# Optimization experiments

Hardware: AMD Instinct MI355X
Metric: run time of the kernel (lower is better)

## Reference

```python
import jax, jax.numpy as jnp
import numpy as np

N_TRAIN = 131072
M_TEST = 65536
T_SPAN = 100.0
D = 3  # Matern-5/2 state dim


def setup_inputs() -> dict:
    key = jax.random.key(0)
    k1, k2, k3, k4 = jax.random.split(key, 4)
    times = jnp.sort(jax.random.uniform(k1, (N_TRAIN,), jnp.float32) * T_SPAN)
    t_star = jnp.sort(jax.random.uniform(k2, (M_TEST,), jnp.float32) * T_SPAN)
    # positive site precisions, site naturals scaled so pseudo-targets are O(1)
    site_nat2 = jax.random.uniform(k3, (N_TRAIN,), jnp.float32) * 4.0 + 0.5
    site_nat1 = jax.random.normal(k4, (N_TRAIN,), jnp.float32) * site_nat2
    return dict(
        times=times,
        t_star=t_star,
        site_nat1=site_nat1,
        site_nat2=site_nat2,
        variance=jnp.float32(1.0),
        lengthscale=jnp.float32(0.5),
        mean_const=jnp.float32(0.1),
    )


def _matern52_sde(variance, lengthscale):
    lam = jnp.sqrt(5.0).astype(jnp.float32) / lengthscale
    F = jnp.array([[0.0, 1.0, 0.0],
                   [0.0, 0.0, 1.0],
                   [0.0, 0.0, 0.0]], jnp.float32)
    F = F.at[2, 0].set(-lam ** 3).at[2, 1].set(-3.0 * lam ** 2).at[2, 2].set(-3.0 * lam)
    kappa = lam ** 2 / 3.0
    P_inf = variance * jnp.array([[1.0, 0.0, 0.0],
                                  [0.0, 0.0, 0.0],
                                  [0.0, 0.0, 0.0]], jnp.float32)
    P_inf = P_inf.at[0, 2].set(-variance * kappa)
    P_inf = P_inf.at[2, 0].set(-variance * kappa)
    P_inf = P_inf.at[1, 1].set(variance * kappa)
    P_inf = P_inf.at[2, 2].set(variance * lam ** 4)
    H = jnp.array([[1.0, 0.0, 0.0]], jnp.float32)
    return F, H, P_inf, lam


def _discretise(F, P_inf, lam, dt):
    # (F + lam I) is nilpotent of index 3 -> exact expm
    I = jnp.eye(D, dtype=jnp.float32)
    Nm = F + lam * I
    Nm2 = Nm @ Nm
    dt_ = dt[:, None, None]
    A = jnp.exp(-lam * dt)[:, None, None] * (I + dt_ * Nm + 0.5 * dt_ ** 2 * Nm2)
    APA = jnp.einsum('tij,jk,tlk->til', A, P_inf, A)
    Q = P_inf - APA
    return A, Q


def _kalman_filter(H, P_inf, A_seq, Q_seq, residual, is_obs, R_full):
    h = H[0]  # [D]

    def step(carry, inp):
        m, P = carry
        A, Q, r, obs, R = inp
        m_pred = A @ m
        P_pred = A @ P @ A.T + Q
        S = h @ P_pred @ h + R
        K = obs * (P_pred @ h) / S  # masked gain: test points skip update
        v = r - m_pred @ h
        m_f = m_pred + K * v
        P_f = P_pred - jnp.outer(K, K) * S
        return (m_f, P_f), (m_pred, P_pred, m_f, P_f)

    init = (jnp.zeros(D, jnp.float32), P_inf)
    _, (m_pred, P_pred, m_filt, P_filt) = jax.lax.scan(
        step, init, (A_seq, Q_seq, residual, is_obs, R_full))
    return m_pred, P_pred, m_filt, P_filt


def _rts_smoother(m_pred, P_pred, m_filt, P_filt, A_seq):
    def back(carry, inp):
        m_s_next, P_s_next = carry
        m_f, P_f, A_n, m_p_n, P_p_n = inp
        G = jnp.linalg.solve(P_p_n, A_n @ P_f).T  # P_f A^T P_pred^{-1}
        m_s = m_f + G @ (m_s_next - m_p_n)
        P_s = P_f + G @ (P_s_next - P_p_n) @ G.T
        return (m_s, P_s), (m_s, P_s)

    init = (m_filt[-1], P_filt[-1])
    xs = (m_filt[:-1], P_filt[:-1], A_seq[1:], m_pred[1:], P_pred[1:])
    _, (m_s, P_s) = jax.lax.scan(back, init, xs, reverse=True)
    m_smooth = jnp.concatenate([m_s, m_filt[-1:]], axis=0)
    P_smooth = jnp.concatenate([P_s, P_filt[-1:]], axis=0)
    return m_smooth, P_smooth


def reference(times, t_star, site_nat1, site_nat2, variance, lengthscale, mean_const):
    F, H, P_inf, lam = _matern52_sde(variance, lengthscale)
    N = times.shape[0]
    M = t_star.shape[0]
    merged = jnp.concatenate([times, t_star])
    order = jnp.argsort(merged)  # jnp.argsort is stable
    merged_sorted = merged[order]
    is_obs = jnp.concatenate([jnp.ones(N, jnp.float32), jnp.zeros(M, jnp.float32)])[order]
    pseudo_targets = site_nat1 / site_nat2
    residual_full = jnp.concatenate([pseudo_targets - mean_const,
                                     jnp.zeros(M, jnp.float32)])[order]
    R_full = jnp.concatenate([jnp.reciprocal(site_nat2), jnp.ones(M, jnp.float32)])[order]
    dt_full = jnp.concatenate([jnp.zeros(1, jnp.float32), jnp.diff(merged_sorted)])
    A_seq, Q_seq = _discretise(F, P_inf, lam, dt_full)
    m_pred, P_pred, m_filt, P_filt = _kalman_filter(
        H, P_inf, A_seq, Q_seq, residual_full, is_obs, R_full)
    m_smooth, P_smooth = _rts_smoother(m_pred, P_pred, m_filt, P_filt, A_seq)
    inv_order = jnp.argsort(order)
    test_positions = inv_order[N:]
    m_test = m_smooth[test_positions]
    P_test = P_smooth[test_positions]
    means = m_test @ H[0] + mean_const  # H = [1,0,0]
    vars_ = jnp.einsum('i,tij,j->t', H[0], P_test, H[0])
    return means, jnp.maximum(vars_, 0.0)
```

## Files before the change

kernel.cpp:

```cpp
#include <hip/hip_runtime.h>
#include <math.h>

#define DEV __device__ __forceinline__

constexpr int N_TRAIN = 131072;
constexpr int M_TEST  = 65536;
constexpr int T_TOT   = N_TRAIN + M_TEST;
constexpr int CHUNK   = 4;
constexpr int NTH     = T_TOT / CHUNK;
constexpr int TPB     = 64;
constexpr int NBLK    = NTH / TPB;
constexpr int MIDT    = 256;
constexpr int FE_S    = 33;
constexpr int SE_S    = 19;

DEV int IDX4(int k) { return (k & (CHUNK - 1)) * NTH + (k >> 2); }

DEV void mm(const double* X, const double* Y, double* Z) {
#pragma unroll
  for (int i = 0; i < 3; ++i)
#pragma unroll
    for (int j = 0; j < 3; ++j)
      Z[i*3+j] = X[i*3]*Y[j] + X[i*3+1]*Y[3+j] + X[i*3+2]*Y[6+j];
}
DEV void mmnt(const double* X, const double* Y, double* Z) {
#pragma unroll
  for (int i = 0; i < 3; ++i)
#pragma unroll
    for (int j = 0; j < 3; ++j)
      Z[i*3+j] = X[i*3]*Y[j*3] + X[i*3+1]*Y[j*3+1] + X[i*3+2]*Y[j*3+2];
}
DEV void mtn(const double* X, const double* Y, double* Z) {
#pragma unroll
  for (int i = 0; i < 3; ++i)
#pragma unroll
    for (int j = 0; j < 3; ++j)
      Z[i*3+j] = X[i]*Y[j] + X[3+i]*Y[3+j] + X[6+i]*Y[6+j];
}
DEV void mv(const double* X, const double* v, double* w) {
#pragma unroll
  for (int i = 0; i < 3; ++i) w[i] = X[i*3]*v[0] + X[i*3+1]*v[1] + X[i*3+2]*v[2];
}
DEV void mtv(const double* X, const double* v, double* w) {
#pragma unroll
  for (int i = 0; i < 3; ++i) w[i] = X[i]*v[0] + X[3+i]*v[1] + X[6+i]*v[2];
}
DEV void inv3(const double* m, double* o) {
  double c00 = m[4]*m[8] - m[5]*m[7];
  double c10 = m[5]*m[6] - m[3]*m[8];
  double c20 = m[3]*m[7] - m[4]*m[6];
  double det = m[0]*c00 + m[1]*c10 + m[2]*c20;
  double id = 1.0 / det;
  o[0] = c00*id; o[1] = (m[2]*m[7]-m[1]*m[8])*id; o[2] = (m[1]*m[5]-m[2]*m[4])*id;
  o[3] = c10*id; o[4] = (m[0]*m[8]-m[2]*m[6])*id; o[5] = (m[2]*m[3]-m[0]*m[5])*id;
  o[6] = c20*id; o[7] = (m[1]*m[6]-m[0]*m[7])*id; o[8] = (m[0]*m[4]-m[1]*m[3])*id;
}
DEV void symm(double* P) {
  double a = 0.5*(P[1]+P[3]), b = 0.5*(P[2]+P[6]), c = 0.5*(P[5]+P[7]);
  P[1]=P[3]=a; P[2]=P[6]=b; P[5]=P[7]=c;
}

struct Model { double lam, v, kap, l4; };
DEV Model make_model(const float* varp, const float* ellp) {
  Model M; M.v = (double)varp[0];
  double ell = (double)ellp[0];
  M.lam = sqrt(5.0) / ell;
  M.kap = M.lam * M.lam / 3.0;
  double l2 = M.lam * M.lam;
  M.l4 = l2 * l2;
  return M;
}
DEV void pinf(const Model& M, double* P) {
  double vk = M.v * M.kap;
  P[0]=M.v; P[1]=0;  P[2]=-vk;
  P[3]=0;   P[4]=vk; P[5]=0;
  P[6]=-vk; P[7]=0;  P[8]=M.v*M.l4;
}
DEV void make_AQ(const Model& M, double dt, double* A, double* Q) {
  double lam = M.lam, l2 = lam*lam, l3 = l2*lam, l4 = M.l4;
  double e = (double)__expf((float)(-lam * dt));
  double h = 0.5 * dt * dt;
  A[0] = e*(1.0 + dt*lam + h*l2);
  A[1] = e*(dt + 2.0*h*lam);
  A[2] = e*h;
  A[3] = e*(-h*l3);
  A[4] = e*(1.0 + dt*lam - 2.0*h*l2);
  A[5] = e*(dt - h*lam);
  A[6] = e*(-dt*l3 + h*l4);
  A[7] = e*(-3.0*dt*l2 + 2.0*h*l3);
  A[8] = e*(1.0 - 2.0*dt*lam + h*l2);
  double vk = M.v * M.kap, vl4 = M.v * M.l4;
  double B[9];
#pragma unroll
  for (int i = 0; i < 3; ++i) {
    B[i*3+0] =  A[i*3+0]*M.v - A[i*3+2]*vk;
    B[i*3+1] =  A[i*3+1]*vk;
    B[i*3+2] = -A[i*3+0]*vk  + A[i*3+2]*vl4;
  }
  double Pi[9]; pinf(M, Pi);
#pragma unroll
  for (int i = 0; i < 3; ++i)
#pragma unroll
    for (int j = 0; j < 3; ++j)
      Q[i*3+j] = Pi[i*3+j] - (B[i*3]*A[j*3] + B[i*3+1]*A[j*3+1] + B[i*3+2]*A[j*3+2]);
}

struct FE { double A[9]; double b[3]; double C[9]; double h[3]; double J[9]; };

DEV FE fe_identity() {
  FE e;
#pragma unroll
  for (int i=0;i<9;++i){ e.A[i]=0.0; e.C[i]=0.0; e.J[i]=0.0; }
  e.A[0]=e.A[4]=e.A[8]=1.0;
  e.b[0]=e.b[1]=e.b[2]=0.0; e.h[0]=e.h[1]=e.h[2]=0.0;
  return e;
}
DEV void fe_store(const FE& e, double* g) {
#pragma unroll
  for (int i=0;i<9;++i) g[i]=e.A[i];
  g[9]=e.b[0]; g[10]=e.b[1]; g[11]=e.b[2];
#pragma unroll
  for (int i=0;i<9;++i) g[12+i]=e.C[i];
  g[21]=e.h[0]; g[22]=e.h[1]; g[23]=e.h[2];
#pragma unroll
  for (int i=0;i<9;++i) g[24+i]=e.J[i];
}
DEV FE fe_load(const double* g) {
  FE e;
#pragma unroll
  for (int i=0;i<9;++i) e.A[i]=g[i];
  e.b[0]=g[9]; e.b[1]=g[10]; e.b[2]=g[11];
#pragma unroll
  for (int i=0;i<9;++i) e.C[i]=g[12+i];
  e.h[0]=g[21]; e.h[1]=g[22]; e.h[2]=g[23];
#pragma unroll
  for (int i=0;i<9;++i) e.J[i]=g[24+i];
  return e;
}
DEV FE build_felem(const Model& M, double dt, float obsf, float rf, float Rf_, bool first) {
  FE E;
  double r = (double)rf, R = (double)Rf_;
  double g = (obsf > 0.5f) ? 1.0 : 0.0;
  if (first) {
#pragma unroll
    for (int i=0;i<9;++i){ E.A[i]=0.0; E.J[i]=0.0; }
    E.h[0]=E.h[1]=E.h[2]=0.0;
    double Pi[9]; pinf(M, Pi);
    double S = Pi[0] + R;
    double f = g / S;
    double K0=Pi[0]*f, K1=Pi[3]*f, K2=Pi[6]*f;
    E.b[0]=K0*r; E.b[1]=K1*r; E.b[2]=K2*r;
    E.C[0]=Pi[0]-S*K0*K0; E.C[1]=Pi[1]-S*K0*K1; E.C[2]=Pi[2]-S*K0*K2;
    E.C[3]=Pi[3]-S*K1*K0; E.C[4]=Pi[4]-S*K1*K1; E.C[5]=Pi[5]-S*K1*K2;
    E.C[6]=Pi[6]-S*K2*K0; E.C[7]=Pi[7]-S*K2*K1; E.C[8]=Pi[8]-S*K2*K2;
    return E;
  }
  double Am[9], Q[9]; make_AQ(M, dt, Am, Q);
  double S = Q[0] + R, iS = g / S;
  double K0=Q[0]*iS, K1=Q[3]*iS, K2=Q[6]*iS;
#pragma unroll
  for (int j = 0; j < 3; ++j) {
    E.A[j]   = Am[j]   - K0*Am[j];
    E.A[3+j] = Am[3+j] - K1*Am[j];
    E.A[6+j] = Am[6+j] - K2*Am[j];
    E.C[j]   = Q[j]    - K0*Q[j];
    E.C[3+j] = Q[3+j]  - K1*Q[j];
    E.C[6+j] = Q[6+j]  - K2*Q[j];
  }
  E.b[0]=K0*r; E.b[1]=K1*r; E.b[2]=K2*r;
  double riS = r*iS;
  E.h[0]=Am[0]*riS; E.h[1]=Am[1]*riS; E.h[2]=Am[2]*riS;
#pragma unroll
  for (int i = 0; i < 3; ++i)
#pragma unroll
    for (int j = 0; j < 3; ++j)
      E.J[i*3+j] = Am[i]*Am[j]*iS;
  return E;
}
DEV FE fcompose(const FE& x, const FE& y) {
  const double *A1=x.A,*b1=x.b,*C1=x.C,*h1=x.h,*J1=x.J;
  const double *A2=y.A,*b2=y.b,*C2=y.C,*h2=y.h,*J2=y.J;
  FE o;
  double Mx[9]; mm(C1,J2,Mx); Mx[0]+=1.0; Mx[4]+=1.0; Mx[8]+=1.0;
  double Mi[9]; inv3(Mx,Mi);
  double T1[9]; mm(A2,Mi,T1);
  mm(T1,A1,o.A);
  double u[3]; mv(C1,h2,u); u[0]+=b1[0]; u[1]+=b1[1]; u[2]+=b1[2];
  mv(T1,u,o.b); o.b[0]+=b2[0]; o.b[1]+=b2[1]; o.b[2]+=b2[2];
  double t2[9]; mm(T1,C1,t2);
  mmnt(t2,A2,o.C);
#pragma unroll
  for (int i=0;i<9;++i) o.C[i]+=C2[i];
  double tmp[9]; mm(Mi,A1,tmp);
  double w[3]; mv(J2,b1,w);
  w[0]=h2[0]-w[0]; w[1]=h2[1]-w[1]; w[2]=h2[2]-w[2];
  mtv(tmp,w,o.h); o.h[0]+=h1[0]; o.h[1]+=h1[1]; o.h[2]+=h1[2];
  double V[9]; mm(J2,A1,V);
  mtn(tmp,V,o.J);
#pragma unroll
  for (int i=0;i<9;++i) o.J[i]+=J1[i];
  symm(o.C); symm(o.J);
  return o;
}
DEV void fstep(const Model& M, double dt, float obsf, float rf, float Rf_,
               double* m, double* P) {
  double A[9], Q[9]; make_AQ(M, dt, A, Q);
  double mp[3]; mv(A, m, mp);
  double W[9]; mmnt(P, A, W);
  double Pp[9]; mm(A, W, Pp);
#pragma unroll
  for (int i=0;i<9;++i) Pp[i]+=Q[i];
  double S = Pp[0] + (double)Rf_;
  double f = (obsf > 0.5f) ? (1.0/S) : 0.0;
  double K0=Pp[0]*f, K1=Pp[3]*f, K2=Pp[6]*f;
  double v = (double)rf - mp[0];
  m[0]=mp[0]+K0*v; m[1]=mp[1]+K1*v; m[2]=mp[2]+K2*v;
  P[0]=Pp[0]-S*K0*K0; P[1]=Pp[1]-S*K0*K1; P[2]=Pp[2]-S*K0*K2;
  P[3]=Pp[3]-S*K1*K0; P[4]=Pp[4]-S*K1*K1; P[5]=Pp[5]-S*K1*K2;
  P[6]=Pp[6]-S*K2*K0; P[7]=Pp[7]-S*K2*K1; P[8]=Pp[8]-S*K2*K2;
  symm(P);
}

struct SE { double G[9]; double c[3]; double U[9]; };

DEV SE se_identity() {
  SE s;
#pragma unroll
  for (int i=0;i<9;++i){ s.G[i]=0.0; s.U[i]=0.0; }
  s.G[0]=s.G[4]=s.G[8]=1.0;
  s.c[0]=s.c[1]=s.c[2]=0.0;
  return s;
}
DEV void se_store(const SE& s, double* g) {
#pragma unroll
  for (int i=0;i<9;++i) g[i]=s.G[i];
  g[9]=s.c[0]; g[10]=s.c[1]; g[11]=s.c[2];
  g[12]=s.U[0]; g[13]=s.U[1]; g[14]=s.U[2]; g[15]=s.U[4]; g[16]=s.U[5]; g[17]=s.U[8];
}
DEV SE se_load(const double* g) {
  SE s;
#pragma unroll
  for (int i=0;i<9;++i) s.G[i]=g[i];
  s.c[0]=g[9]; s.c[1]=g[10]; s.c[2]=g[11];
  s.U[0]=g[12]; s.U[1]=g[13]; s.U[2]=g[14];
  s.U[3]=g[13]; s.U[4]=g[15]; s.U[5]=g[16];
  s.U[6]=g[14]; s.U[7]=g[16]; s.U[8]=g[17];
  return s;
}
DEV SE scompose(const SE& x, const SE& y) {
  SE o;
  mm(x.G, y.G, o.G);
  double t[3]; mv(x.G, y.c, t);
  o.c[0]=t[0]+x.c[0]; o.c[1]=t[1]+x.c[1]; o.c[2]=t[2]+x.c[2];
  double T[9]; mm(x.G, y.U, T);
  mmnt(T, x.G, o.U);
#pragma unroll
  for (int i=0;i<9;++i) o.U[i]+=x.U[i];
  symm(o.U);
  return o;
}
DEV void sapply(const SE& s, double* m, double* P) {
  double t[3]; mv(s.G, m, t);
  double T[9]; mm(s.G, P, T);
  double Pn[9]; mmnt(T, s.G, Pn);
  m[0]=t[0]+s.c[0]; m[1]=t[1]+s.c[1]; m[2]=t[2]+s.c[2];
#pragma unroll
  for (int i=0;i<9;++i) P[i]=Pn[i]+s.U[i];
  symm(P);
}
DEV SE build_selem(const Model& M, const float4* pk, const double* mf, const double* Pf,
                   int i, int t) {
  int ik  = i*NTH + t;
  int ik1 = (i < CHUNK-1) ? (ik + NTH) : (t + 1);
  double m[3] = { mf[ik], mf[T_TOT+ik], mf[2*T_TOT+ik] };
  double p00=Pf[ik], p01=Pf[T_TOT+ik], p02=Pf[2*T_TOT+ik],
         p11=Pf[3*T_TOT+ik], p12=Pf[4*T_TOT+ik], p22=Pf[5*T_TOT+ik];
  double P[9] = { p00,p01,p02, p01,p11,p12, p02,p12,p22 };
  double dt = (double)(pk[ik1].x - pk[ik].x);
  SE s;
  double A[9], Q[9]; make_AQ(M, dt, A, Q);
  double W[9]; mmnt(P, A, W);
  double Pp[9]; mm(A, W, Pp);
#pragma unroll
  for (int j=0;j<9;++j) Pp[j]+=Q[j];
  double Pi_[9]; inv3(Pp, Pi_);
  mm(W, Pi_, s.G);
  double mp[3]; mv(A, m, mp);
  double gm[3]; mv(s.G, mp, gm);
  s.c[0]=m[0]-gm[0]; s.c[1]=m[1]-gm[1]; s.c[2]=m[2]-gm[2];
  double GW[9]; mmnt(s.G, W, GW);
#pragma unroll
  for (int j=0;j<9;++j) s.U[j]=P[j]-GW[j];
  symm(s.U);
  return s;
}

__global__ void k_merge(const float* __restrict__ times, const float* __restrict__ tstar,
                        const float* __restrict__ n1, const float* __restrict__ n2,
                        const float* __restrict__ mcp,
                        float4* pk, int* oix) {
  int g = blockIdx.x*blockDim.x + threadIdx.x;
  if (g >= T_TOT) return;
  float mc = mcp[0];
  if (g < N_TRAIN) {
    int i = g;
    float t = times[i];
    int lo = 0, hi = M_TEST;
    while (lo < hi) { int mid=(lo+hi)>>1; if (tstar[mid] < t) lo=mid+1; else hi=mid; }
    int p = i + lo, ip = IDX4(p);
    float s2 = n2[i];
    pk[ip] = make_float4(t, n1[i]/s2 - mc, 1.0f/s2, 1.0f);
    oix[ip] = -1;
  } else {
    int j = g - N_TRAIN;
    float t = tstar[j];
    int lo = 0, hi = N_TRAIN;
    while (lo < hi) { int mid=(lo+hi)>>1; if (times[mid] <= t) lo=mid+1; else hi=mid; }
    int p = j + lo, ip = IDX4(p);
    pk[ip] = make_float4(t, 0.f, 1.f, 0.f);
    oix[ip] = j;
  }
}

__global__ __launch_bounds__(TPB, 2) void k_f1(
    const float* varp, const float* ellp, const float4* __restrict__ pk,
    double* tIncl, double* blkAgg) {
  __shared__ double lds[TPB*FE_S];
  int l = threadIdx.x, b = blockIdx.x;
  int t = b*TPB + l;
  Model M = make_model(varp, ellp);
  FE run;
  float tprev = (t == 0) ? 0.0f : pk[(CHUNK-1)*NTH + (t-1)].x;
#pragma unroll
  for (int i = 0; i < CHUNK; ++i) {
    float4 q = pk[i*NTH + t];
    bool first = (t==0 && i==0);
    double dt = first ? 0.0 : (double)(q.x - tprev);
    tprev = q.x;
    FE e = build_felem(M, dt, q.w, q.y, q.z, first);
    run = (i == 0) ? e : fcompose(run, e);
  }
  fe_store(run, &lds[l*FE_S]);
  for (int d = 1; d < TPB; d <<= 1) {
    __syncthreads();
    FE oth; bool act = (l >= d);
    if (act) oth = fe_load(&lds[(l-d)*FE_S]);
    __syncthreads();
    if (act) { run = fcompose(oth, run); fe_store(run, &lds[l*FE_S]); }
  }
  fe_store(run, tIncl + t*33);
  if (l == TPB-1) fe_store(run, blkAgg + b*33);
}

__global__ __launch_bounds__(MIDT, 1) void k_f2(const double* __restrict__ blkAgg,
                                                double* blkPref) {
  __shared__ double lds[MIDT*FE_S];
  int j = threadIdx.x;
  FE run;
  {
    FE a0 = fe_load(blkAgg + (3*j+0)*33);
    FE a1 = fe_load(blkAgg + (3*j+1)*33);
    FE a2 = fe_load(blkAgg + (3*j+2)*33);
    run = fcompose(fcompose(a0, a1), a2);
  }
  fe_store(run, &lds[j*FE_S]);
  for (int d = 1; d < MIDT; d <<= 1) {
    __syncthreads();
    FE oth; bool act = (j >= d);
    if (act) oth = fe_load(&lds[(j-d)*FE_S]);
    __syncthreads();
    if (act) { run = fcompose(oth, run); fe_store(run, &lds[j*FE_S]); }
  }
  __syncthreads();
  FE X = (j == 0) ? fe_identity() : fe_load(&lds[(j-1)*FE_S]);
  fe_store(X, blkPref + (3*j+0)*33);
  FE a0 = fe_load(blkAgg + (3*j+0)*33);
  FE x1 = fcompose(X, a0);
  fe_store(x1, blkPref + (3*j+1)*33);
  FE a1 = fe_load(blkAgg + (3*j+1)*33);
  FE x2 = fcompose(x1, a1);
  fe_store(x2, blkPref + (3*j+2)*33);
}

__global__ __launch_bounds__(TPB, 2) void k_f3(
    const float* varp, const float* ellp, const float4* __restrict__ pk,
    const double* __restrict__ tIncl, const double* __restrict__ blkPref,
    double* mf, double* Pf) {
  int l = threadIdx.x, b = blockIdx.x;
  int t = b*TPB + l;
  Model M = make_model(varp, ellp);
  double m[3], P[9];
  if (t == 0) {
    m[0]=m[1]=m[2]=0.0; pinf(M, P);
  } else {
    FE bp = fe_load(blkPref + b*33);
    FE ent = (l == 0) ? bp : fcompose(bp, fe_load(tIncl + (t-1)*33));
    m[0]=ent.b[0]; m[1]=ent.b[1]; m[2]=ent.b[2];
#pragma unroll
    for (int i=0;i<9;++i) P[i]=ent.C[i];
  }
  float tprev = (t == 0) ? 0.0f : pk[(CHUNK-1)*NTH + (t-1)].x;
#pragma unroll
  for (int i = 0; i < CHUNK; ++i) {
    int ik = i*NTH + t;
    float4 q = pk[ik];
    bool first = (t==0 && i==0);
    double dt = first ? 0.0 : (double)(q.x - tprev);
    tprev = q.x;
    fstep(M, dt, q.w, q.y, q.z, m, P);
    mf[ik]=m[0]; mf[T_TOT+ik]=m[1]; mf[2*T_TOT+ik]=m[2];
    Pf[ik]=P[0]; Pf[T_TOT+ik]=P[1]; Pf[2*T_TOT+ik]=P[2];
    Pf[3*T_TOT+ik]=P[4]; Pf[4*T_TOT+ik]=P[5]; Pf[5*T_TOT+ik]=P[8];
  }
}

__global__ __launch_bounds__(TPB, 2) void k_s1(
    const float* varp, const float* ellp, const float4* __restrict__ pk,
    const double* __restrict__ mf, const double* __restrict__ Pf,
    double* tSuf, double* blkAggS) {
  __shared__ double lds[TPB*SE_S];
  int l = threadIdx.x, b = blockIdx.x;
  int t = b*TPB + l;
  Model M = make_model(varp, ellp);
  SE Macc = se_identity();
#pragma unroll
  for (int i = CHUNK-1; i >= 0; --i) {
    int k = t*CHUNK + i;
    if (k <= T_TOT-2) {
      SE e = build_selem(M, pk, mf, Pf, i, t);
      Macc = scompose(e, Macc);
    }
  }
  se_store(Macc, &lds[l*SE_S]);
  for (int d = 1; d < TPB; d <<= 1) {
    __syncthreads();
    SE oth; bool act = (l + d < TPB);
    if (act) oth = se_load(&lds[(l+d)*SE_S]);
    __syncthreads();
    if (act) { Macc = scompose(Macc, oth); se_store(Macc, &lds[l*SE_S]); }
  }
  se_store(Macc, tSuf + t*18);
  if (l == 0) se_store(Macc, blkAggS + b*18);
}

__global__ __launch_bounds__(MIDT, 1) void k_s2(const double* __restrict__ blkAggS,
                                                const double* __restrict__ mf,
                                                const double* __restrict__ Pf,
                                                double* bExit) {
  __shared__ double lds[MIDT*SE_S];
  int j = threadIdx.x;
  SE run;
  {
    SE a0 = se_load(blkAggS + (3*j+0)*18);
    SE a1 = se_load(blkAggS + (3*j+1)*18);
    SE a2 = se_load(blkAggS + (3*j+2)*18);
    run = scompose(a0, scompose(a1, a2));
  }
  se_store(run, &lds[j*SE_S]);
  for (int d = 1; d < MIDT; d <<= 1) {
    __syncthreads();
    SE oth; bool act = (j + d < MIDT);
    if (act) oth = se_load(&lds[(j+d)*SE_S]);
    __syncthreads();
    if (act) { run = scompose(run, oth); se_store(run, &lds[j*SE_S]); }
  }
  __syncthreads();
  int ikF = (CHUNK-1)*NTH + (NTH-1);
  double mT[3] = { mf[ikF], mf[T_TOT+ikF], mf[2*T_TOT+ikF] };
  double p00=Pf[ikF], p01=Pf[T_TOT+ikF], p02=Pf[2*T_TOT+ikF],
         p11=Pf[3*T_TOT+ikF], p12=Pf[4*T_TOT+ikF], p22=Pf[5*T_TOT+ikF];
  double PT[9] = { p00,p01,p02, p01,p11,p12, p02,p12,p22 };
  SE Sx = (j == MIDT-1) ? se_identity() : se_load(&lds[(j+1)*SE_S]);
  SE a1 = se_load(blkAggS + (3*j+1)*18);
  SE a2 = se_load(blkAggS + (3*j+2)*18);
  SE s2x = scompose(a2, Sx);
  SE s1x = scompose(a1, s2x);
  {
    double m[3]={mT[0],mT[1],mT[2]}, P[9];
#pragma unroll
    for (int i=0;i<9;++i) P[i]=PT[i];
    if (j < MIDT-1) sapply(Sx, m, P);
    double* o = bExit + (3*j+2)*9;
    o[0]=m[0];o[1]=m[1];o[2]=m[2];o[3]=P[0];o[4]=P[1];o[5]=P[2];o[6]=P[4];o[7]=P[5];o[8]=P[8];
  }
  {
    double m[3]={mT[0],mT[1],mT[2]}, P[9];
#pragma unroll
    for (int i=0;i<9;++i) P[i]=PT[i];
    sapply(s2x, m, P);
    double* o = bExit + (3*j+1)*9;
    o[0]=m[0];o[1]=m[1];o[2]=m[2];o[3]=P[0];o[4]=P[1];o[5]=P[2];o[6]=P[4];o[7]=P[5];o[8]=P[8];
  }
  {
    double m[3]={mT[0],mT[1],mT[2]}, P[9];
#pragma unroll
    for (int i=0;i<9;++i) P[i]=PT[i];
    sapply(s1x, m, P);
    double* o = bExit + (3*j+0)*9;
    o[0]=m[0];o[1]=m[1];o[2]=m[2];o[3]=P[0];o[4]=P[1];o[5]=P[2];o[6]=P[4];o[7]=P[5];o[8]=P[8];
  }
}

__global__ __launch_bounds__(TPB, 2) void k_s3(
    const float* varp, const float* ellp, const float* mcp,
    const float4* __restrict__ pk,
    const double* __restrict__ mf, const double* __restrict__ Pf,
    const double* __restrict__ tSuf, const double* __restrict__ bExit,
    const int* __restrict__ oix, float* out) {
  int l = threadIdx.x, b = blockIdx.x;
  int t = b*TPB + l;
  Model M = make_model(varp, ellp);
  double mc = (double)mcp[0];
  const double* g = bExit + b*9;
  double m[3] = { g[0], g[1], g[2] };
  double P[9] = { g[3],g[4],g[5], g[4],g[6],g[7], g[5],g[7],g[8] };
  if (l < TPB-1) {
    SE s = se_load(tSuf + (t+1)*18);
    sapply(s, m, P);
  }
  if (t == NTH-1) {
    int ik = (CHUNK-1)*NTH + t;
    int j = oix[ik];
    if (j >= 0) { out[j] = (float)(m[0] + mc); out[M_TEST + j] = (float)fmax(P[0], 0.0); }
  }
#pragma unroll
  for (int i = CHUNK-1; i >= 0; --i) {
    int k = t*CHUNK + i;
    if (k <= T_TOT-2) {
      SE e = build_selem(M, pk, mf, Pf, i, t);
      sapply(e, m, P);
      int ik = i*NTH + t;
      int j = oix[ik];
      if (j >= 0) { out[j] = (float)(m[0] + mc); out[M_TEST + j] = (float)fmax(P[0], 0.0); }
    }
  }
}

extern "C" void kernel_launch(void* const* d_in, const int* in_sizes, int n_in,
                              void* d_out, int out_size, void* d_ws, size_t ws_size,
                              hipStream_t stream) {
  const float* times = (const float*)d_in[0];
  const float* tstar = (const float*)d_in[1];
  const float* n1    = (const float*)d_in[2];
  const float* n2    = (const float*)d_in[3];
  const float* varp  = (const float*)d_in[4];
  const float* ellp  = (const float*)d_in[5];
  const float* mcp   = (const float*)d_in[6];
  float* out = (float*)d_out;

  size_t off = 0;
  auto take = [&](size_t bytes) {
    char* p = (char*)d_ws + off;
    off += (bytes + 255) & ~(size_t)255;
    return (void*)p;
  };
  float4* pk   = (float4*)take(sizeof(float4) * T_TOT);
  int*    oix  = (int*)   take(sizeof(int)    * T_TOT);
  double* mf   = (double*)take(sizeof(double) * 3 * T_TOT);
  double* Pf   = (double*)take(sizeof(double) * 6 * T_TOT);
  double* tIncl= (double*)take(sizeof(double) * 33 * NTH);
  double* blkAgg=(double*)take(sizeof(double) * 33 * NBLK);
  double* blkPref=(double*)take(sizeof(double)* 33 * NBLK);
  double* tSuf = (double*)take(sizeof(double) * 18 * NTH);
  double* blkAggS=(double*)take(sizeof(double)* 18 * NBLK);
  double* bExit= (double*)take(sizeof(double) * 9  * NBLK);
  (void)ws_size; (void)in_sizes; (void)n_in; (void)out_size;

  k_merge<<<(T_TOT+255)/256, 256, 0, stream>>>(times, tstar, n1, n2, mcp, pk, oix);
  k_f1   <<<NBLK, TPB, 0, stream>>>(varp, ellp, pk, tIncl, blkAgg);
  k_f2   <<<1, MIDT, 0, stream>>>(blkAgg, blkPref);
  k_f3   <<<NBLK, TPB, 0, stream>>>(varp, ellp, pk, tIncl, blkPref, mf, Pf);
  k_s1   <<<NBLK, TPB, 0, stream>>>(varp, ellp, pk, mf, Pf, tSuf, blkAggS);
  k_s2   <<<1, MIDT, 0, stream>>>(blkAggS, mf, Pf, bExit);
  k_s3   <<<NBLK, TPB, 0, stream>>>(varp, ellp, mcp, pk, mf, Pf, tSuf, bExit, oix, out);
}
```

Measured before the change: 164.8 us.

## Switch Kalman scan to fp32 and drop per-thread chunking

Converts all scan state, element algebra and workspace buffers from double to float, keeping only the 3x3 inverse in double. It also removes the per-thread chunk of four steps, so each thread handles one time step, which gives four times as many blocks. The middle scan kernels now use 512 threads, each handling six block aggregates, and the final filtered state is passed through a small buffer. The aim is to avoid slow fp64 arithmetic and halve memory traffic, at the risk of losing precision in the long associative compositions.

Result: slower. 218.2 us (+32.4%).

```diff
diff --git a/kernel.cpp b/kernel.cpp
--- a/kernel.cpp
+++ b/kernel.cpp
@@ -6,98 +6,97 @@
 constexpr int N_TRAIN = 131072;
 constexpr int M_TEST  = 65536;
 constexpr int T_TOT   = N_TRAIN + M_TEST;
-constexpr int CHUNK   = 4;
-constexpr int NTH     = T_TOT / CHUNK;
 constexpr int TPB     = 64;
-constexpr int NBLK    = NTH / TPB;
-constexpr int MIDT    = 256;
+constexpr int NBLK    = T_TOT / TPB;
+constexpr int MIDT    = 512;
+constexpr int MPT     = NBLK / MIDT;
 constexpr int FE_S    = 33;
 constexpr int SE_S    = 19;
 
-DEV int IDX4(int k) { return (k & (CHUNK - 1)) * NTH + (k >> 2); }
-
-DEV void mm(const double* X, const double* Y, double* Z) {
+DEV void mm(const float* X, const float* Y, float* Z) {
 #pragma unroll
   for (int i = 0; i < 3; ++i)
 #pragma unroll
     for (int j = 0; j < 3; ++j)
       Z[i*3+j] = X[i*3]*Y[j] + X[i*3+1]*Y[3+j] + X[i*3+2]*Y[6+j];
 }
-DEV void mmnt(const double* X, const double* Y, double* Z) {
+DEV void mmnt(const float* X, const float* Y, float* Z) {
 #pragma unroll
   for (int i = 0; i < 3; ++i)
 #pragma unroll
     for (int j = 0; j < 3; ++j)
       Z[i*3+j] = X[i*3]*Y[j*3] + X[i*3+1]*Y[j*3+1] + X[i*3+2]*Y[j*3+2];
 }
-DEV void mtn(const double* X, const double* Y, double* Z) {
+DEV void mtn(const float* X, const float* Y, float* Z) {
 #pragma unroll
   for (int i = 0; i < 3; ++i)
 #pragma unroll
     for (int j = 0; j < 3; ++j)
       Z[i*3+j] = X[i]*Y[j] + X[3+i]*Y[3+j] + X[6+i]*Y[6+j];
 }
-DEV void mv(const double* X, const double* v, double* w) {
+DEV void mv(const float* X, const float* v, float* w) {
 #pragma unroll
   for (int i = 0; i < 3; ++i) w[i] = X[i*3]*v[0] + X[i*3+1]*v[1] + X[i*3+2]*v[2];
 }
-DEV void mtv(const double* X, const double* v, double* w) {
+DEV void mtv(const float* X, const float* v, float* w) {
 #pragma unroll
   for (int i = 0; i < 3; ++i) w[i] = X[i]*v[0] + X[3+i]*v[1] + X[6+i]*v[2];
 }
-DEV void inv3(const double* m, double* o) {
-  double c00 = m[4]*m[8] - m[5]*m[7];
-  double c10 = m[5]*m[6] - m[3]*m[8];
-  double c20 = m[3]*m[7] - m[4]*m[6];
-  double det = m[0]*c00 + m[1]*c10 + m[2]*c20;
+DEV void inv3(const float* mf_, float* o) {
+  double m0=mf_[0], m1=mf_[1], m2=mf_[2], m3=mf_[3], m4=mf_[4],
+         m5=mf_[5], m6=mf_[6], m7=mf_[7], m8=mf_[8];
+  double c00 = m4*m8 - m5*m7;
+  double c10 = m5*m6 - m3*m8;
+  double c20 = m3*m7 - m4*m6;
+  double det = m0*c00 + m1*c10 + m2*c20;
   double id = 1.0 / det;
-  o[0] = c00*id; o[1] = (m[2]*m[7]-m[1]*m[8])*id; o[2] = (m[1]*m[5]-m[2]*m[4])*id;
-  o[3] = c10*id; o[4] = (m[0]*m[8]-m[2]*m[6])*id; o[5] = (m[2]*m[3]-m[0]*m[5])*id;
-  o[6] = c20*id; o[7] = (m[1]*m[6]-m[0]*m[7])*id; o[8] = (m[0]*m[4]-m[1]*m[3])*id;
-}
-DEV void symm(double* P) {
-  double a = 0.5*(P[1]+P[3]), b = 0.5*(P[2]+P[6]), c = 0.5*(P[5]+P[7]);
+  o[0] = (float)(c00*id); o[1] = (float)((m2*m7-m1*m8)*id); o[2] = (float)((m1*m5-m2*m4)*id);
+  o[3] = (float)(c10*id); o[4] = (float)((m0*m8-m2*m6)*id); o[5] = (float)((m2*m3-m0*m5)*id);
+  o[6] = (float)(c20*id); o[7] = (float)((m1*m6-m0*m7)*id); o[8] = (float)((m0*m4-m1*m3)*id);
+}
+DEV void symm(float* P) {
+  float a = 0.5f*(P[1]+P[3]), b = 0.5f*(P[2]+P[6]), c = 0.5f*(P[5]+P[7]);
   P[1]=P[3]=a; P[2]=P[6]=b; P[5]=P[7]=c;
 }
 
-struct Model { double lam, v, kap, l4; };
+struct Model { float lam, v, kap, l4; };
 DEV Model make_model(const float* varp, const float* ellp) {
-  Model M; M.v = (double)varp[0];
-  double ell = (double)ellp[0];
-  M.lam = sqrt(5.0) / ell;
-  M.kap = M.lam * M.lam / 3.0;
-  double l2 = M.lam * M.lam;
+  Model M; M.v = varp[0];
+  float ell = ellp[0];
+  M.lam = sqrtf(5.0f) / ell;
+  M.kap = M.lam * M.lam / 3.0f;
+  float l2 = M.lam * M.lam;
   M.l4 = l2 * l2;
   return M;
 }
-DEV void pinf(const Model& M, double* P) {
-  double vk = M.v * M.kap;
+DEV void pinf(const Model& M, float* P) {
+  float vk = M.v * M.kap;
   P[0]=M.v; P[1]=0;  P[2]=-vk;
   P[3]=0;   P[4]=vk; P[5]=0;
   P[6]=-vk; P[7]=0;  P[8]=M.v*M.l4;
 }
-DEV void make_AQ(const Model& M, double dt, double* A, double* Q) {
-  double lam = M.lam, l2 = lam*lam, l3 = l2*lam, l4 = M.l4;
-  double e = (double)__expf((float)(-lam * dt));
-  double h = 0.5 * dt * dt;
-  A[0] = e*(1.0 + dt*lam + h*l2);
-  A[1] = e*(dt + 2.0*h*lam);
+DEV void make_AQ(const Model& M, float dt, float* A, float* Q) {
+  float lam = M.lam, l2 = lam*lam, l3 = l2*lam, l4 = M.l4;
+  float e = __expf(-lam * dt);
+  float h = 0.5f * dt * dt;
+  A[0] = e*(1.0f + dt*lam + h*l2);
+  A[1] = e*(dt + 2.0f*h*lam);
   A[2] = e*h;
   A[3] = e*(-h*l3);
-  A[4] = e*(1.0 + dt*lam - 2.0*h*l2);
+  A[4] = e*(1.0f + dt*lam - 2.0f*h*l2);
   A[5] = e*(dt - h*lam);
   A[6] = e*(-dt*l3 + h*l4);
-  A[7] = e*(-3.0*dt*l2 + 2.0*h*l3);
-  A[8] = e*(1.0 - 2.0*dt*lam + h*l2);
-  double vk = M.v * M.kap, vl4 = M.v * M.l4;
-  double B[9];
+  A[7] = e*(-3.0f*dt*l2 + 2.0f*h*l3);
+  A[8] = e*(1.0f - 2.0f*dt*lam + h*l2);
+  float vk = M.v * M.kap, vl4 = M.v * M.l4;
+  float B[9];
 #pragma unroll
   for (int i = 0; i < 3; ++i) {
     B[i*3+0] =  A[i*3+0]*M.v - A[i*3+2]*vk;
     B[i*3+1] =  A[i*3+1]*vk;
     B[i*3+2] = -A[i*3+0]*vk  + A[i*3+2]*vl4;
   }
-  double Pi[9]; pinf(M, Pi);
+  float Pi[9]; pinf(M, Pi);
 #pragma unroll
   for (int i = 0; i < 3; ++i)
 #pragma unroll
@@ -105,17 +104,17 @@
       Q[i*3+j] = Pi[i*3+j] - (B[i*3]*A[j*3] + B[i*3+1]*A[j*3+1] + B[i*3+2]*A[j*3+2]);
 }
 
-struct FE { double A[9]; double b[3]; double C[9]; double h[3]; double J[9]; };
+struct FE { float A[9]; float b[3]; float C[9]; float h[3]; float J[9]; };
 
 DEV FE fe_identity() {
   FE e;
 #pragma unroll
-  for (int i=0;i<9;++i){ e.A[i]=0.0; e.C[i]=0.0; e.J[i]=0.0; }
-  e.A[0]=e.A[4]=e.A[8]=1.0;
-  e.b[0]=e.b[1]=e.b[2]=0.0; e.h[0]=e.h[1]=e.h[2]=0.0;
+  for (int i=0;i<9;++i){ e.A[i]=0.0f; e.C[i]=0.0f; e.J[i]=0.0f; }
+  e.A[0]=e.A[4]=e.A[8]=1.0f;
+  e.b[0]=e.b[1]=e.b[2]=0.0f; e.h[0]=e.h[1]=e.h[2]=0.0f;
   return e;
 }
-DEV void fe_store(const FE& e, double* g) {
+DEV void fe_store(const FE& e, float* g) {
 #pragma unroll
   for (int i=0;i<9;++i) g[i]=e.A[i];
   g[9]=e.b[0]; g[10]=e.b[1]; g[11]=e.b[2];
@@ -125,7 +124,7 @@
 #pragma unroll
   for (int i=0;i<9;++i) g[24+i]=e.J[i];
 }
-DEV FE fe_load(const double* g) {
+DEV FE fe_load(const float* g) {
   FE e;
 #pragma unroll
   for (int i=0;i<9;++i) e.A[i]=g[i];
@@ -137,27 +136,27 @@
   for (int i=0;i<9;++i) e.J[i]=g[24+i];
   return e;
 }
-DEV FE build_felem(const Model& M, double dt, float obsf, float rf, float Rf_, bool first) {
+DEV FE build_felem(const Model& M, float dt, float obsf, float rf, float Rf_, bool first) {
   FE E;
-  double r = (double)rf, R = (double)Rf_;
-  double g = (obsf > 0.5f) ? 1.0 : 0.0;
+  float r = rf, R = Rf_;
+  float g = (obsf > 0.5f) ? 1.0f : 0.0f;
   if (first) {
 #pragma unroll
-    for (int i=0;i<9;++i){ E.A[i]=0.0; E.J[i]=0.0; }
-    E.h[0]=E.h[1]=E.h[2]=0.0;
-    double Pi[9]; pinf(M, Pi);
-    double S = Pi[0] + R;
-    double f = g / S;
-    double K0=Pi[0]*f, K1=Pi[3]*f, K2=Pi[6]*f;
+    for (int i=0;i<9;++i){ E.A[i]=0.0f; E.J[i]=0.0f; }
+    E.h[0]=E.h[1]=E.h[2]=0.0f;
+    float Pi[9]; pinf(M, Pi);
+    float S = Pi[0] + R;
+    float f = g / S;
+    float K0=Pi[0]*f, K1=Pi[3]*f, K2=Pi[6]*f;
     E.b[0]=K0*r; E.b[1]=K1*r; E.b[2]=K2*r;
     E.C[0]=Pi[0]-S*K0*K0; E.C[1]=Pi[1]-S*K0*K1; E.C[2]=Pi[2]-S*K0*K2;
     E.C[3]=Pi[3]-S*K1*K0; E.C[4]=Pi[4]-S*K1*K1; E.C[5]=Pi[5]-S*K1*K2;
     E.C[6]=Pi[6]-S*K2*K0; E.C[7]=Pi[7]-S*K2*K1; E.C[8]=Pi[8]-S*K2*K2;
     return E;
   }
-  double Am[9], Q[9]; make_AQ(M, dt, Am, Q);
-  double S = Q[0] + R, iS = g / S;
-  double K0=Q[0]*iS, K1=Q[3]*iS, K2=Q[6]*iS;
+  float Am[9], Q[9]; make_AQ(M, dt, Am, Q);
+  float S = Q[0] + R, iS = g / S;
+  float K0=Q[0]*iS, K1=Q[3]*iS, K2=Q[6]*iS;
 #pragma unroll
   for (int j = 0; j < 3; ++j) {
     E.A[j]   = Am[j]   - K0*Am[j];
@@ -168,7 +167,7 @@
     E.C[6+j] = Q[6+j]  - K2*Q[j];
   }
   E.b[0]=K0*r; E.b[1]=K1*r; E.b[2]=K2*r;
-  double riS = r*iS;
+  float riS = r*iS;
   E.h[0]=Am[0]*riS; E.h[1]=Am[1]*riS; E.h[2]=Am[2]*riS;
 #pragma unroll
   for (int i = 0; i < 3; ++i)
@@ -178,42 +177,42 @@
   return E;
 }
 DEV FE fcompose(const FE& x, const FE& y) {
-  const double *A1=x.A,*b1=x.b,*C1=x.C,*h1=x.h,*J1=x.J;
-  const double *A2=y.A,*b2=y.b,*C2=y.C,*h2=y.h,*J2=y.J;
+  const float *A1=x.A,*b1=x.b,*C1=x.C,*h1=x.h,*J1=x.J;
+  const float *A2=y.A,*b2=y.b,*C2=y.C,*h2=y.h,*J2=y.J;
   FE o;
-  double Mx[9]; mm(C1,J2,Mx); Mx[0]+=1.0; Mx[4]+=1.0; Mx[8]+=1.0;
-  double Mi[9]; inv3(Mx,Mi);
-  double T1[9]; mm(A2,Mi,T1);
+  float Mx[9]; mm(C1,J2,Mx); Mx[0]+=1.0f; Mx[4]+=1.0f; Mx[8]+=1.0f;
+  float Mi[9]; inv3(Mx,Mi);
+  float T1[9]; mm(A2,Mi,T1);
   mm(T1,A1,o.A);
-  double u[3]; mv(C1,h2,u); u[0]+=b1[0]; u[1]+=b1[1]; u[2]+=b1[2];
+  float u[3]; mv(C1,h2,u); u[0]+=b1[0]; u[1]+=b1[1]; u[2]+=b1[2];
   mv(T1,u,o.b); o.b[0]+=b2[0]; o.b[1]+=b2[1]; o.b[2]+=b2[2];
-  double t2[9]; mm(T1,C1,t2);
+  float t2[9]; mm(T1,C1,t2);
   mmnt(t2,A2,o.C);
 #pragma unroll
   for (int i=0;i<9;++i) o.C[i]+=C2[i];
-  double tmp[9]; mm(Mi,A1,tmp);
-  double w[3]; mv(J2,b1,w);
+  float tmp[9]; mm(Mi,A1,tmp);
+  float w[3]; mv(J2,b1,w);
   w[0]=h2[0]-w[0]; w[1]=h2[1]-w[1]; w[2]=h2[2]-w[2];
   mtv(tmp,w,o.h); o.h[0]+=h1[0]; o.h[1]+=h1[1]; o.h[2]+=h1[2];
-  double V[9]; mm(J2,A1,V);
+  float V[9]; mm(J2,A1,V);
   mtn(tmp,V,o.J);
 #pragma unroll
   for (int i=0;i<9;++i) o.J[i]+=J1[i];
   symm(o.C); symm(o.J);
   return o;
 }
-DEV void fstep(const Model& M, double dt, float obsf, float rf, float Rf_,
-               double* m, double* P) {
-  double A[9], Q[9]; make_AQ(M, dt, A, Q);
-  double mp[3]; mv(A, m, mp);
-  double W[9]; mmnt(P, A, W);
-  double Pp[9]; mm(A, W, Pp);
+DEV void fstep(const Model& M, float dt, float obsf, float rf, float Rf_,
+               float* m, float* P) {
+  float A[9], Q[9]; make_AQ(M, dt, A, Q);
+  float mp[3]; mv(A, m, mp);
+  float W[9]; mmnt(P, A, W);
+  float Pp[9]; mm(A, W, Pp);
 #pragma unroll
   for (int i=0;i<9;++i) Pp[i]+=Q[i];
-  double S = Pp[0] + (double)Rf_;
-  double f = (obsf > 0.5f) ? (1.0/S) : 0.0;
-  double K0=Pp[0]*f, K1=Pp[3]*f, K2=Pp[6]*f;
-  double v = (double)rf - mp[0];
+  float S = Pp[0] + Rf_;
+  float f = (obsf > 0.5f) ? (1.0f/S) : 0.0f;
+  float K0=Pp[0]*f, K1=Pp[3]*f, K2=Pp[6]*f;
+  float v = rf - mp[0];
   m[0]=mp[0]+K0*v; m[1]=mp[1]+K1*v; m[2]=mp[2]+K2*v;
   P[0]=Pp[0]-S*K0*K0; P[1]=Pp[1]-S*K0*K1; P[2]=Pp[2]-S*K0*K2;
   P[3]=Pp[3]-S*K1*K0; P[4]=Pp[4]-S*K1*K1; P[5]=Pp[5]-S*K1*K2;
@@ -221,23 +220,23 @@
   symm(P);
 }
 
-struct SE { double G[9]; double c[3]; double U[9]; };
+struct SE { float G[9]; float c[3]; float U[9]; };
 
 DEV SE se_identity() {
   SE s;
 #pragma unroll
-  for (int i=0;i<9;++i){ s.G[i]=0.0; s.U[i]=0.0; }
-  s.G[0]=s.G[4]=s.G[8]=1.0;
-  s.c[0]=s.c[1]=s.c[2]=0.0;
+  for (int i=0;i<9;++i){ s.G[i]=0.0f; s.U[i]=0.0f; }
+  s.G[0]=s.G[4]=s.G[8]=1.0f;
+  s.c[0]=s.c[1]=s.c[2]=0.0f;
   return s;
 }
-DEV void se_store(const SE& s, double* g) {
+DEV void se_store(const SE& s, float* g) {
 #pragma unroll
   for (int i=0;i<9;++i) g[i]=s.G[i];
   g[9]=s.c[0]; g[10]=s.c[1]; g[11]=s.c[2];
   g[12]=s.U[0]; g[13]=s.U[1]; g[14]=s.U[2]; g[15]=s.U[4]; g[16]=s.U[5]; g[17]=s.U[8];
 }
-DEV SE se_load(const double* g) {
+DEV SE se_load(const float* g) {
   SE s;
 #pragma unroll
   for (int i=0;i<9;++i) s.G[i]=g[i];
@@ -250,45 +249,42 @@
 DEV SE scompose(const SE& x, const SE& y) {
   SE o;
   mm(x.G, y.G, o.G);
-  double t[3]; mv(x.G, y.c, t);
+  float t[3]; mv(x.G, y.c, t);
   o.c[0]=t[0]+x.c[0]; o.c[1]=t[1]+x.c[1]; o.c[2]=t[2]+x.c[2];
-  double T[9]; mm(x.G, y.U, T);
+  float T[9]; mm(x.G, y.U, T);
   mmnt(T, x.G, o.U);
 #pragma unroll
   for (int i=0;i<9;++i) o.U[i]+=x.U[i];
   symm(o.U);
   return o;
 }
-DEV void sapply(const SE& s, double* m, double* P) {
-  double t[3]; mv(s.G, m, t);
-  double T[9]; mm(s.G, P, T);
-  double Pn[9]; mmnt(T, s.G, Pn);
+DEV void sapply(const SE& s, float* m, float* P) {
+  float t[3]; mv(s.G, m, t);
+  float T[9]; mm(s.G, P, T);
+  float Pn[9]; mmnt(T, s.G, Pn);
   m[0]=t[0]+s.c[0]; m[1]=t[1]+s.c[1]; m[2]=t[2]+s.c[2];
 #pragma unroll
   for (int i=0;i<9;++i) P[i]=Pn[i]+s.U[i];
   symm(P);
 }
-DEV SE build_selem(const Model& M, const float4* pk, const double* mf, const double* Pf,
-                   int i, int t) {
-  int ik  = i*NTH + t;
-  int ik1 = (i < CHUNK-1) ? (ik + NTH) : (t + 1);
-  double m[3] = { mf[ik], mf[T_TOT+ik], mf[2*T_TOT+ik] };
-  double p00=Pf[ik], p01=Pf[T_TOT+ik], p02=Pf[2*T_TOT+ik],
-         p11=Pf[3*T_TOT+ik], p12=Pf[4*T_TOT+ik], p22=Pf[5*T_TOT+ik];
-  double P[9] = { p00,p01,p02, p01,p11,p12, p02,p12,p22 };
-  double dt = (double)(pk[ik1].x - pk[ik].x);
+DEV SE build_selem(const Model& M, const float4* pk, const float* mf, const float* Pf, int k) {
+  float m[3] = { mf[k], mf[T_TOT+k], mf[2*T_TOT+k] };
+  float p00=Pf[k], p01=Pf[T_TOT+k], p02=Pf[2*T_TOT+k],
+        p11=Pf[3*T_TOT+k], p12=Pf[4*T_TOT+k], p22=Pf[5*T_TOT+k];
+  float P[9] = { p00,p01,p02, p01,p11,p12, p02,p12,p22 };
+  float dt = pk[k+1].x - pk[k].x;
   SE s;
-  double A[9], Q[9]; make_AQ(M, dt, A, Q);
-  double W[9]; mmnt(P, A, W);
-  double Pp[9]; mm(A, W, Pp);
+  float A[9], Q[9]; make_AQ(M, dt, A, Q);
+  float W[9]; mmnt(P, A, W);
+  float Pp[9]; mm(A, W, Pp);
 #pragma unroll
   for (int j=0;j<9;++j) Pp[j]+=Q[j];
-  double Pi_[9]; inv3(Pp, Pi_);
+  float Pi_[9]; inv3(Pp, Pi_);
   mm(W, Pi_, s.G);
-  double mp[3]; mv(A, m, mp);
-  double gm[3]; mv(s.G, mp, gm);
+  float mp[3]; mv(A, m, mp);
+  float gm[3]; mv(s.G, mp, gm);
   s.c[0]=m[0]-gm[0]; s.c[1]=m[1]-gm[1]; s.c[2]=m[2]-gm[2];
-  double GW[9]; mmnt(s.G, W, GW);
+  float GW[9]; mmnt(s.G, W, GW);
 #pragma unroll
   for (int j=0;j<9;++j) s.U[j]=P[j]-GW[j];
   symm(s.U);
@@ -307,39 +303,31 @@
     float t = times[i];
     int lo = 0, hi = M_TEST;
     while (lo < hi) { int mid=(lo+hi)>>1; if (tstar[mid] < t) lo=mid+1; else hi=mid; }
-    int p = i + lo, ip = IDX4(p);
+    int p = i + lo;
     float s2 = n2[i];
-    pk[ip] = make_float4(t, n1[i]/s2 - mc, 1.0f/s2, 1.0f);
-    oix[ip] = -1;
+    pk[p] = make_float4(t, n1[i]/s2 - mc, 1.0f/s2, 1.0f);
+    oix[p] = -1;
   } else {
     int j = g - N_TRAIN;
     float t = tstar[j];
     int lo = 0, hi = N_TRAIN;
     while (lo < hi) { int mid=(lo+hi)>>1; if (times[mid] <= t) lo=mid+1; else hi=mid; }
-    int p = j + lo, ip = IDX4(p);
-    pk[ip] = make_float4(t, 0.f, 1.f, 0.f);
-    oix[ip] = j;
-  }
-}
-
-__global__ __launch_bounds__(TPB, 2) void k_f1(
+    int p = j + lo;
+    pk[p] = make_float4(t, 0.f, 1.f, 0.f);
+    oix[p] = j;
+  }
+}
+
+__global__ __launch_bounds__(TPB, 3) void k_f1(
     const float* varp, const float* ellp, const float4* __restrict__ pk,
-    double* tIncl, double* blkAgg) {
-  __shared__ double lds[TPB*FE_S];
+    float* tIncl, float* blkAgg) {
+  __shared__ float lds[TPB*FE_S];
   int l = threadIdx.x, b = blockIdx.x;
   int t = b*TPB + l;
   Model M = make_model(varp, ellp);
-  FE run;
-  float tprev = (t == 0) ? 0.0f : pk[(CHUNK-1)*NTH + (t-1)].x;
-#pragma unroll
-  for (int i = 0; i < CHUNK; ++i) {
-    float4 q = pk[i*NTH + t];
-    bool first = (t==0 && i==0);
-    double dt = first ? 0.0 : (double)(q.x - tprev);
-    tprev = q.x;
-    FE e = build_felem(M, dt, q.w, q.y, q.z, first);
-    run = (i == 0) ? e : fcompose(run, e);
-  }
+  float4 q = pk[t];
+  float dt = (t == 0) ? 0.0f : (q.x - pk[t-1].x);
+  FE run = build_felem(M, dt, q.w, q.y, q.z, t == 0);
   fe_store(run, &lds[l*FE_S]);
   for (int d = 1; d < TPB; d <<= 1) {
     __syncthreads();
@@ -348,21 +336,17 @@
     __syncthreads();
     if (act) { run = fcompose(oth, run); fe_store(run, &lds[l*FE_S]); }
   }
-  fe_store(run, tIncl + t*33);
-  if (l == TPB-1) fe_store(run, blkAgg + b*33);
-}
-
-__global__ __launch_bounds__(MIDT, 1) void k_f2(const double* __restrict__ blkAgg,
-                                                double* blkPref) {
-  __shared__ double lds[MIDT*FE_S];
+  fe_store(run, tIncl + t*FE_S);
+  if (l == TPB-1) fe_store(run, blkAgg + b*FE_S);
+}
+
+__global__ __launch_bounds__(MIDT, 2) void k_f2(const float* __restrict__ blkAgg,
+                                                float* blkPref) {
+  __shared__ float lds[MIDT*FE_S];
   int j = threadIdx.x;
-  FE run;
-  {
-    FE a0 = fe_load(blkAgg + (3*j+0)*33);
-    FE a1 = fe_load(blkAgg + (3*j+1)*33);
-    FE a2 = fe_load(blkAgg + (3*j+2)*33);
-    run = fcompose(fcompose(a0, a1), a2);
-  }
+  FE run = fe_load(blkAgg + (MPT*j)*FE_S);
+#pragma unroll
+  for (int i = 1; i < MPT; ++i) run = fcompose(run, fe_load(blkAgg + (MPT*j+i)*FE_S));
   fe_store(run, &lds[j*FE_S]);
   for (int d = 1; d < MIDT; d <<= 1) {
     __syncthreads();
@@ -373,64 +357,53 @@
   }
   __syncthreads();
   FE X = (j == 0) ? fe_identity() : fe_load(&lds[(j-1)*FE_S]);
-  fe_store(X, blkPref + (3*j+0)*33);
-  FE a0 = fe_load(blkAgg + (3*j+0)*33);
-  FE x1 = fcompose(X, a0);
-  fe_store(x1, blkPref + (3*j+1)*33);
-  FE a1 = fe_load(blkAgg + (3*j+1)*33);
-  FE x2 = fcompose(x1, a1);
-  fe_store(x2, blkPref + (3*j+2)*33);
-}
-
-__global__ __launch_bounds__(TPB, 2) void k_f3(
+  fe_store(X, blkPref + (MPT*j)*FE_S);
+#pragma unroll
+  for (int i = 0; i < MPT-1; ++i) {
+    X = fcompose(X, fe_load(blkAgg + (MPT*j+i)*FE_S));
+    fe_store(X, blkPref + (MPT*j+i+1)*FE_S);
+  }
+}
+
+__global__ __launch_bounds__(TPB, 3) void k_f3(
     const float* varp, const float* ellp, const float4* __restrict__ pk,
-    const double* __restrict__ tIncl, const double* __restrict__ blkPref,
-    double* mf, double* Pf) {
+    const float* __restrict__ tIncl, const float* __restrict__ blkPref,
+    float* mf, float* Pf, float* xT) {
   int l = threadIdx.x, b = blockIdx.x;
   int t = b*TPB + l;
   Model M = make_model(varp, ellp);
-  double m[3], P[9];
+  float m[3], P[9];
   if (t == 0) {
-    m[0]=m[1]=m[2]=0.0; pinf(M, P);
+    m[0]=m[1]=m[2]=0.0f; pinf(M, P);
   } else {
-    FE bp = fe_load(blkPref + b*33);
-    FE ent = (l == 0) ? bp : fcompose(bp, fe_load(tIncl + (t-1)*33));
+    FE bp = fe_load(blkPref + b*FE_S);
+    FE ent = (l == 0) ? bp : fcompose(bp, fe_load(tIncl + (t-1)*FE_S));
     m[0]=ent.b[0]; m[1]=ent.b[1]; m[2]=ent.b[2];
 #pragma unroll
     for (int i=0;i<9;++i) P[i]=ent.C[i];
   }
-  float tprev = (t == 0) ? 0.0f : pk[(CHUNK-1)*NTH + (t-1)].x;
-#pragma unroll
-  for (int i = 0; i < CHUNK; ++i) {
-    int ik = i*NTH + t;
-    float4 q = pk[ik];
-    bool first = (t==0 && i==0);
-    double dt = first ? 0.0 : (double)(q.x - tprev);
-    tprev = q.x;
-    fstep(M, dt, q.w, q.y, q.z, m, P);
-    mf[ik]=m[0]; mf[T_TOT+ik]=m[1]; mf[2*T_TOT+ik]=m[2];
-    Pf[ik]=P[0]; Pf[T_TOT+ik]=P[1]; Pf[2*T_TOT+ik]=P[2];
-    Pf[3*T_TOT+ik]=P[4]; Pf[4*T_TOT+ik]=P[5]; Pf[5*T_TOT+ik]=P[8];
-  }
-}
-
-__global__ __launch_bounds__(TPB, 2) void k_s1(
+  float4 q = pk[t];
+  float dt = (t == 0) ? 0.0f : (q.x - pk[t-1].x);
+  fstep(M, dt, q.w, q.y, q.z, m, P);
+  mf[t]=m[0]; mf[T_TOT+t]=m[1]; mf[2*T_TOT+t]=m[2];
+  Pf[t]=P[0]; Pf[T_TOT+t]=P[1]; Pf[2*T_TOT+t]=P[2];
+  Pf[3*T_TOT+t]=P[4]; Pf[4*T_TOT+t]=P[5]; Pf[5*T_TOT+t]=P[8];
+  if (t == T_TOT-1) {
+    xT[0]=m[0]; xT[1]=m[1]; xT[2]=m[2];
+    xT[3]=P[0]; xT[4]=P[1]; xT[5]=P[2];
+    xT[6]=P[4]; xT[7]=P[5]; xT[8]=P[8];
+  }
+}
+
+__global__ __launch_bounds__(TPB, 3) void k_s1(
     const float* varp, const float* ellp, const float4* __restrict__ pk,
-    const double* __restrict__ mf, const double* __restrict__ Pf,
-    double* tSuf, double* blkAggS) {
-  __shared__ double lds[TPB*SE_S];
+    const float* __restrict__ mf, const float* __restrict__ Pf,
+    float* tSuf, float* blkAggS) {
+  __shared__ float lds[TPB*SE_S];
   int l = threadIdx.x, b = blockIdx.x;
   int t = b*TPB + l;
   Model M = make_model(varp, ellp);
-  SE Macc = se_identity();
-#pragma unroll
-  for (int i = CHUNK-1; i >= 0; --i) {
-    int k = t*CHUNK + i;
-    if (k <= T_TOT-2) {
-      SE e = build_selem(M, pk, mf, Pf, i, t);
-      Macc = scompose(e, Macc);
-    }
-  }
+  SE Macc = (t <= T_TOT-2) ? build_selem(M, pk, mf, Pf, t) : se_identity();
   se_store(Macc, &lds[l*SE_S]);
   for (int d = 1; d < TPB; d <<= 1) {
     __syncthreads();
@@ -443,19 +416,17 @@
   if (l == 0) se_store(Macc, blkAggS + b*18);
 }
 
-__global__ __launch_bounds__(MIDT, 1) void k_s2(const double* __restrict__ blkAggS,
-                                                const double* __restrict__ mf,
-                                                const double* __restrict__ Pf,
-                                                double* bExit) {
-  __shared__ double lds[MIDT*SE_S];
+__global__ __launch_bounds__(MIDT, 2) void k_s2(const float* __restrict__ blkAggS,
+                                                const float* __restrict__ xT,
+                                                float* bExit) {
+  __shared__ float lds[MIDT*SE_S];
   int j = threadIdx.x;
-  SE run;
-  {
-    SE a0 = se_load(blkAggS + (3*j+0)*18);
-    SE a1 = se_load(blkAggS + (3*j+1)*18);
-    SE a2 = se_load(blkAggS + (3*j+2)*18);
-    run = scompose(a0, scompose(a1, a2));
-  }
+  SE a[MPT];
+#pragma unroll
+  for (int i = 0; i < MPT; ++i) a[i] = se_load(blkAggS + (MPT*j+i)*18);
+  SE run = a[MPT-1];
+#pragma unroll
+  for (int i = MPT-2; i >= 0; --i) run = scompose(a[i], run);
   se_store(run, &lds[j*SE_S]);
   for (int d = 1; d < MIDT; d <<= 1) {
     __syncthreads();
@@ -465,75 +436,47 @@
     if (act) { run = scompose(run, oth); se_store(run, &lds[j*SE_S]); }
   }
   __syncthreads();
-  int ikF = (CHUNK-1)*NTH + (NTH-1);
-  double mT[3] = { mf[ikF], mf[T_TOT+ikF], mf[2*T_TOT+ikF] };
-  double p00=Pf[ikF], p01=Pf[T_TOT+ikF], p02=Pf[2*T_TOT+ikF],
-         p11=Pf[3*T_TOT+ikF], p12=Pf[4*T_TOT+ikF], p22=Pf[5*T_TOT+ikF];
-  double PT[9] = { p00,p01,p02, p01,p11,p12, p02,p12,p22 };
-  SE Sx = (j == MIDT-1) ? se_identity() : se_load(&lds[(j+1)*SE_S]);
-  SE a1 = se_load(blkAggS + (3*j+1)*18);
-  SE a2 = se_load(blkAggS + (3*j+2)*18);
-  SE s2x = scompose(a2, Sx);
-  SE s1x = scompose(a1, s2x);
+  float m[3] = { xT[0], xT[1], xT[2] };
+  float P[9] = { xT[3],xT[4],xT[5], xT[4],xT[6],xT[7], xT[5],xT[7],xT[8] };
+  if (j < MIDT-1) {
+    SE Sx = se_load(&lds[(j+1)*SE_S]);
+    sapply(Sx, m, P);
+  }
   {
-    double m[3]={mT[0],mT[1],mT[2]}, P[9];
-#pragma unroll
-    for (int i=0;i<9;++i) P[i]=PT[i];
-    if (j < MIDT-1) sapply(Sx, m, P);
-    double* o = bExit + (3*j+2)*9;
+    float* o = bExit + (MPT*j+MPT-1)*9;
     o[0]=m[0];o[1]=m[1];o[2]=m[2];o[3]=P[0];o[4]=P[1];o[5]=P[2];o[6]=P[4];o[7]=P[5];o[8]=P[8];
   }
-  {
-    double m[3]={mT[0],mT[1],mT[2]}, P[9];
-#pragma unroll
-    for (int i=0;i<9;++i) P[i]=PT[i];
-    sapply(s2x, m, P);
-    double* o = bExit + (3*j+1)*9;
+#pragma unroll
+  for (int i = MPT-1; i >= 1; --i) {
+    sapply(a[i], m, P);
+    float* o = bExit + (MPT*j+i-1)*9;
     o[0]=m[0];o[1]=m[1];o[2]=m[2];o[3]=P[0];o[4]=P[1];o[5]=P[2];o[6]=P[4];o[7]=P[5];o[8]=P[8];
   }
-  {
-    double m[3]={mT[0],mT[1],mT[2]}, P[9];
-#pragma unroll
-    for (int i=0;i<9;++i) P[i]=PT[i];
-    sapply(s1x, m, P);
-    double* o = bExit + (3*j+0)*9;
-    o[0]=m[0];o[1]=m[1];o[2]=m[2];o[3]=P[0];o[4]=P[1];o[5]=P[2];o[6]=P[4];o[7]=P[5];o[8]=P[8];
-  }
-}
-
-__global__ __launch_bounds__(TPB, 2) void k_s3(
+}
+
+__global__ __launch_bounds__(TPB, 3) void k_s3(
     const float* varp, const float* ellp, const float* mcp,
     const float4* __restrict__ pk,
-    const double* __restrict__ mf, const double* __restrict__ Pf,
-    const double* __restrict__ tSuf, const double* __restrict__ bExit,
+    const float* __restrict__ mf, const float* __restrict__ Pf,
+    const float* __restrict__ tSuf, const float* __restrict__ bExit,
     const int* __restrict__ oix, float* out) {
   int l = threadIdx.x, b = blockIdx.x;
   int t = b*TPB + l;
   Model M = make_model(varp, ellp);
-  double mc = (double)mcp[0];
-  const double* g = bExit + b*9;
-  double m[3] = { g[0], g[1], g[2] };
-  double P[9] = { g[3],g[4],g[5], g[4],g[6],g[7], g[5],g[7],g[8] };
+  float mc = mcp[0];
+  const float* g = bExit + b*9;
+  float m[3] = { g[0], g[1], g[2] };
+  float P[9] = { g[3],g[4],g[5], g[4],g[6],g[7], g[5],g[7],g[8] };
   if (l < TPB-1) {
     SE s = se_load(tSuf + (t+1)*18);
     sapply(s, m, P);
   }
-  if (t == NTH-1) {
-    int ik = (CHUNK-1)*NTH + t;
-    int j = oix[ik];
-    if (j >= 0) { out[j] = (float)(m[0] + mc); out[M_TEST + j] = (float)fmax(P[0], 0.0); }
-  }
-#pragma unroll
-  for (int i = CHUNK-1; i >= 0; --i) {
-    int k = t*CHUNK + i;
-    if (k <= T_TOT-2) {
-      SE e = build_selem(M, pk, mf, Pf, i, t);
-      sapply(e, m, P);
-      int ik = i*NTH + t;
-      int j = oix[ik];
-      if (j >= 0) { out[j] = (float)(m[0] + mc); out[M_TEST + j] = (float)fmax(P[0], 0.0); }
-    }
-  }
+  if (t <= T_TOT-2) {
+    SE e = build_selem(M, pk, mf, Pf, t);
+    sapply(e, m, P);
+  }
+  int j = oix[t];
+  if (j >= 0) { out[j] = m[0] + mc; out[M_TEST + j] = fmaxf(P[0], 0.0f); }
 }
 
 extern "C" void kernel_launch(void* const* d_in, const int* in_sizes, int n_in,
@@ -554,23 +497,24 @@
     off += (bytes + 255) & ~(size_t)255;
     return (void*)p;
   };
-  float4* pk   = (float4*)take(sizeof(float4) * T_TOT);
-  int*    oix  = (int*)   take(sizeof(int)    * T_TOT);
-  double* mf   = (double*)take(sizeof(double) * 3 * T_TOT);
-  double* Pf   = (double*)take(sizeof(double) * 6 * T_TOT);
-  double* tIncl= (double*)take(sizeof(double) * 33 * NTH);
-  double* blkAgg=(double*)take(sizeof(double) * 33 * NBLK);
-  double* blkPref=(double*)take(sizeof(double)* 33 * NBLK);
-  double* tSuf = (double*)take(sizeof(double) * 18 * NTH);
-  double* blkAggS=(double*)take(sizeof(double)* 18 * NBLK);
-  double* bExit= (double*)take(sizeof(double) * 9  * NBLK);
+  float4* pk    = (float4*)take(sizeof(float4) * T_TOT);
+  int*    oix   = (int*)   take(sizeof(int)    * T_TOT);
+  float*  mf    = (float*) take(sizeof(float)  * 3 * T_TOT);
+  float*  Pf    = (float*) take(sizeof(float)  * 6 * T_TOT);
+  float*  tIncl = (float*) take(sizeof(float)  * FE_S * T_TOT);
+  float*  blkAgg= (float*) take(sizeof(float)  * FE_S * NBLK);
+  float*  blkPref=(float*) take(sizeof(float)  * FE_S * NBLK);
+  float*  tSuf  = (float*) take(sizeof(float)  * 18 * T_TOT);
+  float*  blkAggS=(float*) take(sizeof(float)  * 18 * NBLK);
+  float*  bExit = (float*) take(sizeof(float)  * 9  * NBLK);
+  float*  xT    = (float*) take(sizeof(float)  * 9);
   (void)ws_size; (void)in_sizes; (void)n_in; (void)out_size;
 
   k_merge<<<(T_TOT+255)/256, 256, 0, stream>>>(times, tstar, n1, n2, mcp, pk, oix);
   k_f1   <<<NBLK, TPB, 0, stream>>>(varp, ellp, pk, tIncl, blkAgg);
   k_f2   <<<1, MIDT, 0, stream>>>(blkAgg, blkPref);
-  k_f3   <<<NBLK, TPB, 0, stream>>>(varp, ellp, pk, tIncl, blkPref, mf, Pf);
+  k_f3   <<<NBLK, TPB, 0, stream>>>(varp, ellp, pk, tIncl, blkPref, mf, Pf, xT);
   k_s1   <<<NBLK, TPB, 0, stream>>>(varp, ellp, pk, mf, Pf, tSuf, blkAggS);
-  k_s2   <<<1, MIDT, 0, stream>>>(blkAggS, mf, Pf, bExit);
+  k_s2   <<<1, MIDT, 0, stream>>>(blkAggS, xT, bExit);
   k_s3   <<<NBLK, TPB, 0, stream>>>(varp, ellp, mcp, pk, mf, Pf, tSuf, bExit, oix, out);
 }
```
